# Optimization experiments

Hardware: AMD Instinct MI355X
Metric: run time of the kernel (lower is better)

Reference implementation:

```python
import jax, jax.numpy as jnp
import numpy as np

GX, GY, NH = 480, 360, 32
EPS = 1e-5


def _bn(x, g, b):
    # torch BatchNorm1d training-mode stats over the point dimension
    m = jnp.mean(x, axis=0)
    v = jnp.mean((x - m) ** 2, axis=0)
    return g * (x - m) / jnp.sqrt(v + EPS) + b


def setup_inputs():
    key = jax.random.key(0)
    ks = jax.random.split(key, 24)
    B, N, F = 2, 120000, 7
    s = 0.02
    inp = {
        "pt_fea": jax.random.normal(ks[0], (B, N, F), jnp.float32),
        "xy_ind": jax.random.randint(ks[1], (B, N, 2), 0, 360, dtype=jnp.int32),
        "bn0_g": jnp.ones((7,), jnp.float32), "bn0_b": jnp.zeros((7,), jnp.float32),
        "W1": jax.random.normal(ks[2], (7, 64), jnp.float32) * s,  "b1": jnp.zeros((64,), jnp.float32),
        "bn1_g": jnp.ones((64,), jnp.float32), "bn1_b": jnp.zeros((64,), jnp.float32),
        "W2": jax.random.normal(ks[3], (64, 128), jnp.float32) * s, "b2": jnp.zeros((128,), jnp.float32),
        "bn2_g": jnp.ones((128,), jnp.float32), "bn2_b": jnp.zeros((128,), jnp.float32),
        "W3": jax.random.normal(ks[4], (128, 256), jnp.float32) * s, "b3": jnp.zeros((256,), jnp.float32),
        "bn3_g": jnp.ones((256,), jnp.float32), "bn3_b": jnp.zeros((256,), jnp.float32),
        "W4": jax.random.normal(ks[5], (256, 512), jnp.float32) * s, "b4": jnp.zeros((512,), jnp.float32),
        "W5": jax.random.normal(ks[6], (512, NH), jnp.float32) * s, "b5": jnp.zeros((NH,), jnp.float32),
    }
    return inp


def _forward_sample(fea, xy, bn0_g, bn0_b, W1, b1, bn1_g, bn1_b, W2, b2,
                    bn2_g, bn2_b, W3, b3, bn3_g, bn3_b, W4, b4, W5, b5):
    # Simplified PointNet: BN -> (Linear, BN, ReLU) x3 -> Linear
    x = _bn(fea, bn0_g, bn0_b)
    x = jax.nn.relu(_bn(x @ W1 + b1, bn1_g, bn1_b))
    x = jax.nn.relu(_bn(x @ W2 + b2, bn2_g, bn2_b))
    x = jax.nn.relu(_bn(x @ W3 + b3, bn3_g, bn3_b))
    x = x @ W4 + b4                              # [N, 512]
    # per-voxel segment max over flattened BEV cell id
    ids = xy[:, 0] * GY + xy[:, 1]               # [N]
    nseg = GX * GY
    seg = jax.ops.segment_max(x, ids, num_segments=nseg)   # [nseg, 512]
    cnt = jax.ops.segment_sum(jnp.ones(ids.shape[0], x.dtype), ids, num_segments=nseg)
    occ = (cnt > 0)[:, None]
    seg = jnp.where(occ, seg, 0.0)               # empty voxels -> 0 (scatter semantics)
    nh = jax.nn.relu(seg @ W5 + b5)              # fea_compression
    nh = jnp.where(occ, nh, 0.0)
    return nh.reshape(GX, GY, NH).transpose(2, 0, 1)  # [NH, GX, GY]


def reference(pt_fea, xy_ind, bn0_g, bn0_b, W1, b1, bn1_g, bn1_b, W2, b2,
              bn2_g, bn2_b, W3, b3, bn3_g, bn3_b, W4, b4, W5, b5):
    f = lambda fea, xy: _forward_sample(fea, xy, bn0_g, bn0_b, W1, b1, bn1_g, bn1_b,
                                        W2, b2, bn2_g, bn2_b, W3, b3, bn3_g, bn3_b,
                                        W4, b4, W5, b5)
    return jax.vmap(f)(pt_fea, xy_ind)           # [B, NH, GX, GY]
```

## Files before the change

### kernel.cpp

```cpp
#include <hip/hip_runtime.h>
#include <cstdint>

#define GXD 480
#define GYD 360
#define NHD 32
#define NPTS 120000
#define MPAD 120064
#define SEGR 129600
#define NSEG (GXD*GYD)
#define EPSB 1e-5f

using short8 = __attribute__((ext_vector_type(8))) short;
using f32x4  = __attribute__((ext_vector_type(4))) float;

__device__ __forceinline__ float bf2f(unsigned short u) {
    return __uint_as_float(((unsigned int)u) << 16);
}
__device__ __forceinline__ unsigned short f2bf(float f) {
    unsigned int u = __float_as_uint(f);
    u += 0x7fffu + ((u >> 16) & 1u);
    return (unsigned short)(u >> 16);
}
__device__ __forceinline__ unsigned int bnrelu_pack(unsigned int wv, float sc0, float sh0,
                                                    float sc1, float sh1)
{
    float lo = __uint_as_float(wv << 16);
    float hi = __uint_as_float(wv & 0xffff0000u);
    lo = fmaxf(fmaf(lo, sc0, sh0), 0.f);
    hi = fmaxf(fmaf(hi, sc1, sh1), 0.f);
    unsigned int r;
    asm("v_cvt_pk_bf16_f32 %0, %1, %2" : "=v"(r) : "v"(lo), "v"(hi));
    return r;
}

__device__ __forceinline__ void async16(const unsigned short* g, unsigned short* l)
{
    __builtin_amdgcn_global_load_lds(
        (const __attribute__((address_space(1))) unsigned int*)g,
        (__attribute__((address_space(3))) unsigned int*)l, 16, 0, 0);
}

__global__ __launch_bounds__(256) void bn0_stats_kernel(
    const float* __restrict__ fea, float* __restrict__ s0, float* __restrict__ q0)
{
    float s[7] = {0,0,0,0,0,0,0}, q[7] = {0,0,0,0,0,0,0};
    for (int p = blockIdx.x * 256 + threadIdx.x; p < NPTS; p += gridDim.x * 256) {
        const float* r = fea + (size_t)p * 7;
#pragma unroll
        for (int f = 0; f < 7; ++f) { float v = r[f]; s[f] += v; q[f] += v * v; }
    }
    __shared__ float red[256];
    int t = threadIdx.x;
#pragma unroll
    for (int f = 0; f < 7; ++f) {
        red[t] = s[f]; __syncthreads();
        for (int o = 128; o > 0; o >>= 1) {
            if (t < o) red[t] += red[t + o];
            __syncthreads();
        }
        if (t == 0) atomicAdd(&s0[f], red[0]);
        __syncthreads();
        red[t] = q[f]; __syncthreads();
        for (int o = 128; o > 0; o >>= 1) {
            if (t < o) red[t] += red[t + o];
            __syncthreads();
        }
        if (t == 0) atomicAdd(&q0[f], red[0]);
        __syncthreads();
    }
}

__global__ void prep0_kernel(const float* __restrict__ s0, const float* __restrict__ q0,
                             const float* __restrict__ g0, const float* __restrict__ b0,
                             const float* __restrict__ W1, const float* __restrict__ b1,
                             float* __restrict__ W1p, float* __restrict__ b1p)
{
    __shared__ float sc[7], sh[7];
    int t = threadIdx.x;
    if (t < 7) {
        float m = s0[t] / (float)NPTS;
        float v = q0[t] / (float)NPTS - m * m;
        float inv = 1.0f / sqrtf(fmaxf(v, 0.f) + EPSB);
        sc[t] = g0[t] * inv;
        sh[t] = b0[t] - m * g0[t] * inv;
    }
    __syncthreads();
    if (t < 64) {
        float acc = b1[t];
#pragma unroll
        for (int f = 0; f < 7; ++f) {
            W1p[f * 64 + t] = W1[f * 64 + t] * sc[f];
            acc += sh[f] * W1[f * 64 + t];
        }
        b1p[t] = acc;
    }
}

__global__ void prep_bn_kernel(const float* __restrict__ sum, const float* __restrict__ sq,
                               const float* __restrict__ g, const float* __restrict__ b,
                               float* __restrict__ sc, float* __restrict__ sh, int C)
{
    int c = blockIdx.x * blockDim.x + threadIdx.x;
    if (c < C) {
        float m = sum[c] / (float)NPTS;
        float v = sq[c] / (float)NPTS - m * m;
        float inv = 1.0f / sqrtf(fmaxf(v, 0.f) + EPSB);
        sc[c] = g[c] * inv;
        sh[c] = b[c] - m * g[c] * inv;
    }
}

template<int C>
__global__ __launch_bounds__(256) void bnrelu_kernel(
    unsigned short* __restrict__ Y,
    const float* __restrict__ sc, const float* __restrict__ sh)
{
    __shared__ float scs[C], shs[C];
    int t = threadIdx.x;
    for (int i = t; i < C; i += 256) { scs[i] = sc[i]; shs[i] = sh[i]; }
    __syncthreads();
    const size_t total8 = (size_t)MPAD * C / 8;
    for (size_t i = (size_t)blockIdx.x * 256 + t; i < total8; i += (size_t)gridDim.x * 256) {
        int c0 = (int)((i * 8) & (size_t)(C - 1));
        uint4 v = *(const uint4*)(Y + i * 8);
        float4 s0 = *(const float4*)&scs[c0];
        float4 s1 = *(const float4*)&scs[c0 + 4];
        float4 h0 = *(const float4*)&shs[c0];
        float4 h1 = *(const float4*)&shs[c0 + 4];
        uint4 o;
        o.x = bnrelu_pack(v.x, s0.x, h0.x, s0.y, h0.y);
        o.y = bnrelu_pack(v.y, s0.z, h0.z, s0.w, h0.w);
        o.z = bnrelu_pack(v.z, s1.x, h1.x, s1.y, h1.y);
        o.w = bnrelu_pack(v.w, s1.z, h1.z, s1.w, h1.w);
        *(uint4*)(Y + i * 8) = o;
    }
}

__global__ __launch_bounds__(256) void wtrans_kernel(const float* __restrict__ W,
                                                     unsigned short* __restrict__ Wt,
                                                     int K, int N)
{
    int i = blockIdx.x * 256 + threadIdx.x;
    if (i < K * N) {
        int k = i / N, n = i % N;
        Wt[(size_t)n * K + k] = f2bf(W[i]);
    }
}

__global__ __launch_bounds__(256) void layer1_kernel(
    const float* __restrict__ fea, const float* __restrict__ W1p, const float* __restrict__ b1p,
    unsigned short* __restrict__ y1, float* __restrict__ sum1, float* __restrict__ sq1)
{
    __shared__ float Wl[448], bl[64];
    __shared__ float feaL[256 * 7];
    __shared__ float colsum[64], colsq[64];
    int t = threadIdx.x;
    int p0 = blockIdx.x * 256;
    for (int i = t; i < 448; i += 256) Wl[i] = W1p[i];
    if (t < 64) { bl[t] = b1p[t]; colsum[t] = 0.f; colsq[t] = 0.f; }
    int nval7 = (NPTS - p0) * 7;
    for (int i = t; i < 256 * 7; i += 256)
        feaL[i] = (i < nval7) ? fea[(size_t)p0 * 7 + i] : 0.f;
    __syncthreads();
    int cg = t & 7, pt = t >> 3;
    float s[8] = {}, q[8] = {};
#pragma unroll
    for (int it = 0; it < 8; ++it) {
        int row = it * 32 + pt;
        bool valid = (p0 + row) < NPTS;
        float f[7];
#pragma unroll
        for (int ff = 0; ff < 7; ++ff) f[ff] = feaL[row * 7 + ff];
        float vj[8];
#pragma unroll
        for (int j = 0; j < 8; ++j) {
            int c = cg * 8 + j;
            float v = bl[c];
#pragma unroll
            for (int ff = 0; ff < 7; ++ff) v = fmaf(f[ff], Wl[ff * 64 + c], v);
            vj[j] = v;
            if (valid) { s[j] += v; q[j] += v * v; }
        }
        uint4 ow;
        ow.x = (unsigned int)f2bf(vj[0]) | ((unsigned int)f2bf(vj[1]) << 16);
        ow.y = (unsigned int)f2bf(vj[2]) | ((unsigned int)f2bf(vj[3]) << 16);
        ow.z = (unsigned int)f2bf(vj[4]) | ((unsigned int)f2bf(vj[5]) << 16);
        ow.w = (unsigned int)f2bf(vj[6]) | ((unsigned int)f2bf(vj[7]) << 16);
        *(uint4*)(y1 + (size_t)(p0 + row) * 64 + cg * 8) = ow;
    }
#pragma unroll
    for (int off = 8; off < 64; off <<= 1) {
#pragma unroll
        for (int j = 0; j < 8; ++j) {
            s[j] += __shfl_xor(s[j], off);
            q[j] += __shfl_xor(q[j], off);
        }
    }
    if ((t & 63) < 8) {
#pragma unroll
        for (int j = 0; j < 8; ++j) {
            atomicAdd(&colsum[cg * 8 + j], s[j]);
            atomicAdd(&colsq[cg * 8 + j], q[j]);
        }
    }
    __syncthreads();
    if (t < 64) {
        atomicAdd(&sum1[t], colsum[t]);
        atomicAdd(&sq1[t], colsq[t]);
    }
}

template<int K, int NC, bool STATS>
__global__ __launch_bounds__(256) void gemm_quad(
    const unsigned short* __restrict__ A, const unsigned short* __restrict__ Wt,
    const float* __restrict__ bias, unsigned short* __restrict__ Y,
    float* __restrict__ osum, float* __restrict__ osq)
{
    __shared__ __align__(16) unsigned short lds[16384];
    __shared__ float colsum[128], colsq[128];
    int t = threadIdx.x;
    int w = t >> 6, ln = t & 63, quad = ln >> 4, lr = ln & 15;
    int wr = w >> 1, wc = w & 1;
    const int mbase = blockIdx.y * 128;
    const int cbase = blockIdx.x * 128;
    unsigned short* Asl = lds;
    unsigned short* Bsl = lds + 8192;

    if (STATS && t < 128) { colsum[t] = 0.f; colsq[t] = 0.f; }
    __syncthreads();

    const int srow = w * 16 + (ln >> 2);
    const int koff = (ln & 3) * 8;

    auto stage = [&](int buf, int kt) {
#pragma unroll
        for (int half = 0; half < 2; ++half) {
            int row = half * 64 + srow;
            async16(A  + (size_t)(mbase + row) * K + kt + koff,
                    Asl + buf * 4096 + half * 2048 + w * 512 + ln * 8);
            async16(Wt + (size_t)(cbase + row) * K + kt + koff,
                    Bsl + buf * 4096 + half * 2048 + w * 512 + ln * 8);
        }
    };

    f32x4 acc[4][4];
#pragma unroll
    for (int i = 0; i < 4; ++i)
#pragma unroll
        for (int j = 0; j < 4; ++j) acc[i][j] = (f32x4){0.f, 0.f, 0.f, 0.f};

    stage(0, 0);
    stage(1, 32);

    constexpr int NR = K / 32;
#pragma unroll
    for (int r = 0; r < NR; ++r) {
        const int buf = r & 1;
        if (r + 1 < NR)
            asm volatile("s_waitcnt vmcnt(4)" ::: "memory");
        else
            asm volatile("s_waitcnt vmcnt(0)" ::: "memory");
        asm volatile("s_barrier" ::: "memory");
        short8 af[4], bfr[4];
#pragma unroll
        for (int mi = 0; mi < 4; ++mi)
            af[mi] = *(const short8*)&Asl[buf * 4096 + (wr * 64 + mi * 16 + lr) * 32 + quad * 8];
#pragma unroll
        for (int ni = 0; ni < 4; ++ni)
            bfr[ni] = *(const short8*)&Bsl[buf * 4096 + (wc * 64 + ni * 16 + lr) * 32 + quad * 8];
        asm volatile("s_waitcnt lgkmcnt(0)" ::: "memory");
        asm volatile("s_barrier" ::: "memory");
        if (r + 2 < NR)
            stage(buf, (r + 2) * 32);
#pragma unroll
        for (int mi = 0; mi < 4; ++mi)
#pragma unroll
            for (int ni = 0; ni < 4; ++ni)
                acc[mi][ni] = __builtin_amdgcn_mfma_f32_16x16x32_bf16(
                    af[mi], bfr[ni], acc[mi][ni], 0, 0, 0);
    }
    __syncthreads();

    unsigned short* Cw = lds + w * 4096;
#pragma unroll
    for (int ni = 0; ni < 4; ++ni) {
        int col = ni * 16 + lr;
        float bv = bias[cbase + wc * 64 + col];
        float s = 0.f, q = 0.f;
#pragma unroll
        for (int mi = 0; mi < 4; ++mi) {
            int rb = mi * 16 + quad * 4;
#pragma unroll
            for (int r = 0; r < 4; ++r) {
                float v = acc[mi][ni][r] + bv;
                Cw[(rb + r) * 64 + col] = f2bf(v);
                if (STATS && (mbase + wr * 64 + rb + r) < NPTS) { s += v; q += v * v; }
            }
        }
        if (STATS) {
            atomicAdd(&colsum[wc * 64 + col], s);
            atomicAdd(&colsq[wc * 64 + col], q);
        }
    }
#pragma unroll
    for (int i = 0; i < 8; ++i) {
        int idx = i * 64 + ln;
        int row = idx >> 3, colq = (idx & 7) * 8;
        *(uint4*)(Y + (size_t)(mbase + wr * 64 + row) * NC + cbase + wc * 64 + colq) =
            *(const uint4*)&Cw[row * 64 + colq];
    }
    if (STATS) {
        __syncthreads();
        if (t < 128) {
            atomicAdd(&osum[blockIdx.x * 128 + t], colsum[t]);
            atomicAdd(&osq[blockIdx.x * 128 + t], colsq[t]);
        }
    }
}

__global__ __launch_bounds__(256) void hist_kernel(const int* __restrict__ xy,
                                                   int* __restrict__ cnt)
{
    int p = blockIdx.x * 256 + threadIdx.x;
    if (p < NPTS) {
        int id = xy[(size_t)p * 2] * GYD + xy[(size_t)p * 2 + 1];
        atomicAdd(&cnt[id], 1);
    }
}

__global__ __launch_bounds__(256) void scanA_kernel(const int* __restrict__ cnt,
                                                    int* __restrict__ csum)
{
    __shared__ int red[256];
    int t = threadIdx.x, base = blockIdx.x * 2048;
    int s = 0;
    for (int i = t; i < 2048; i += 256) {
        int idx = base + i;
        if (idx < SEGR) s += cnt[idx];
    }
    red[t] = s; __syncthreads();
    for (int o = 128; o > 0; o >>= 1) { if (t < o) red[t] += red[t + o]; __syncthreads(); }
    if (t == 0) csum[blockIdx.x] = red[0];
}

__global__ void scanB_kernel(int* __restrict__ csum, int* __restrict__ offs)
{
    if (threadIdx.x == 0) {
        int run = 0;
        for (int i = 0; i < 64; ++i) { int v = csum[i]; csum[i] = run; run += v; }
        offs[SEGR] = run;
    }
}

__global__ __launch_bounds__(256) void scanC_kernel(const int* __restrict__ cnt,
                                                    const int* __restrict__ csum,
                                                    int* __restrict__ offs,
                                                    int* __restrict__ cursor)
{
    __shared__ int red[256];
    int t = threadIdx.x, base = blockIdx.x * 2048;
    int v[8]; int s = 0;
#pragma unroll
    for (int i = 0; i < 8; ++i) {
        int idx = base + t * 8 + i;
        v[i] = (idx < SEGR) ? cnt[idx] : 0;
        s += v[i];
    }
    red[t] = s; __syncthreads();
    for (int o = 1; o < 256; o <<= 1) {
        int x = (t >= o) ? red[t - o] : 0;
        __syncthreads();
        red[t] += x;
        __syncthreads();
    }
    int run = red[t] - s + csum[blockIdx.x];
#pragma unroll
    for (int i = 0; i < 8; ++i) {
        int idx = base + t * 8 + i;
        if (idx < SEGR) { offs[idx] = run; cursor[idx] = run; }
        run += v[i];
    }
}

__global__ __launch_bounds__(256) void scatter_idx_kernel(const int* __restrict__ xy,
                                                          int* __restrict__ cursor,
                                                          int* __restrict__ order)
{
    int p = blockIdx.x * 256 + threadIdx.x;
    if (p < NPTS) {
        int id = xy[(size_t)p * 2] * GYD + xy[(size_t)p * 2 + 1];
        int pos = atomicAdd(&cursor[id], 1);
        order[pos] = p;
    }
}

__global__ __launch_bounds__(256) void segmax_l5_kernel(
    const unsigned short* __restrict__ y4g, const unsigned short* __restrict__ Wt5,
    const int* __restrict__ offs, const int* __restrict__ order,
    int g, float* __restrict__ E)
{
    __shared__ __align__(16) unsigned short seg[64 * 136];
    __shared__ __align__(16) unsigned short w5s[32 * 136];
    __shared__ int offs_s[65];
    int t = threadIdx.x;
    int c0 = blockIdx.x * 64;
    if (t < 65) offs_s[t] = offs[c0 + t];
    {
        int n = t >> 3, ko = (t & 7) * 16;
        *(uint4*)&w5s[n * 136 + ko]     = *(const uint4*)(Wt5 + (size_t)n * 512 + g * 128 + ko);
        *(uint4*)&w5s[n * 136 + ko + 8] = *(const uint4*)(Wt5 + (size_t)n * 512 + g * 128 + ko + 8);
    }
    __syncthreads();
    int cell = t >> 2, q = t & 3;
    float mx[32];
#pragma unroll
    for (int i = 0; i < 32; ++i) mx[i] = -3.0e38f;
    int jb = offs_s[cell], je = offs_s[cell + 1];
    for (int j = jb; j < je; ++j) {
        int p = order[j];
        const uint4* rp = (const uint4*)(y4g + (size_t)p * 128 + q * 32);
#pragma unroll
        for (int u = 0; u < 4; ++u) {
            uint4 vv = rp[u];
            unsigned int wv[4] = {vv.x, vv.y, vv.z, vv.w};
#pragma unroll
            for (int k2 = 0; k2 < 4; ++k2) {
                int idx = u * 8 + k2 * 2;
                mx[idx]     = fmaxf(mx[idx],     bf2f((unsigned short)(wv[k2] & 0xffffu)));
                mx[idx + 1] = fmaxf(mx[idx + 1], bf2f((unsigned short)(wv[k2] >> 16)));
            }
        }
    }
    bool empty = (jb == je);
#pragma unroll
    for (int i = 0; i < 16; ++i) {
        float lo = empty ? 0.f : mx[2 * i], hi = empty ? 0.f : mx[2 * i + 1];
        unsigned int pk = (unsigned int)f2bf(lo) | ((unsigned int)f2bf(hi) << 16);
        *(unsigned int*)&seg[cell * 136 + q * 32 + 2 * i] = pk;
    }
    __syncthreads();
    int lane = t & 63, w = t >> 6, quad = lane >> 4, lr = lane & 15;
    f32x4 acc[2];
    acc[0] = (f32x4){0.f, 0.f, 0.f, 0.f};
    acc[1] = (f32x4){0.f, 0.f, 0.f, 0.f};
#pragma unroll
    for (int kt = 0; kt < 4; ++kt) {
        short8 af = *(const short8*)&seg[(w * 16 + lr) * 136 + kt * 32 + quad * 8];
#pragma unroll
        for (int ni = 0; ni < 2; ++ni) {
            short8 bfr = *(const short8*)&w5s[(ni * 16 + lr) * 136 + kt * 32 + quad * 8];
            acc[ni] = __builtin_amdgcn_mfma_f32_16x16x32_bf16(af, bfr, acc[ni], 0, 0, 0);
        }
    }
#pragma unroll
    for (int ni = 0; ni < 2; ++ni) {
        int h = ni * 16 + lr;
#pragma unroll
        for (int r = 0; r < 4; ++r) {
            int cr = w * 16 + quad * 4 + r;
            float* ep = E + (size_t)(c0 + cr) * 32 + h;
            float v = acc[ni][r];
            if (g > 0) v += *ep;
            *ep = v;
        }
    }
}

__global__ __launch_bounds__(256) void out_kernel(
    const float* __restrict__ E, const int* __restrict__ cnt,
    const float* __restrict__ b5, float* __restrict__ out)
{
    int t = threadIdx.x;
    int c0 = blockIdx.x * 64;
    int lane = t & 63, hq = t >> 6;
    int cell = c0 + lane;
    if (c0 >= SEGR) {
#pragma unroll
        for (int j = 0; j < 8; ++j)
            out[(size_t)(hq * 8 + j) * NSEG + cell] = 0.f;
        return;
    }
    bool oc = cnt[cell] > 0;
    float4 e0 = *(const float4*)(E + (size_t)cell * 32 + hq * 8);
    float4 e1 = *(const float4*)(E + (size_t)cell * 32 + hq * 8 + 4);
    float r[8] = {e0.x, e0.y, e0.z, e0.w, e1.x, e1.y, e1.z, e1.w};
#pragma unroll
    for (int j = 0; j < 8; ++j) {
        float v = oc ? fmaxf(r[j] + b5[hq * 8 + j], 0.f) : 0.f;
        out[(size_t)(hq * 8 + j) * NSEG + cell] = v;
    }
}

extern "C" void kernel_launch(void* const* d_in, const int* in_sizes, int n_in,
                              void* d_out, int out_size, void* d_ws, size_t ws_size,
                              hipStream_t stream)
{
    const float* pt_fea = (const float*)d_in[0];
    const int*   xy_ind = (const int*)d_in[1];
    const float* bn0_g  = (const float*)d_in[2];
    const float* bn0_b  = (const float*)d_in[3];
    const float* W1     = (const float*)d_in[4];
    const float* b1     = (const float*)d_in[5];
    const float* bn1_g  = (const float*)d_in[6];
    const float* bn1_b  = (const float*)d_in[7];
    const float* W2     = (const float*)d_in[8];
    const float* b2     = (const float*)d_in[9];
    const float* bn2_g  = (const float*)d_in[10];
    const float* bn2_b  = (const float*)d_in[11];
    const float* W3     = (const float*)d_in[12];
    const float* b3     = (const float*)d_in[13];
    const float* bn3_g  = (const float*)d_in[14];
    const float* bn3_b  = (const float*)d_in[15];
    const float* W4     = (const float*)d_in[16];
    const float* b4     = (const float*)d_in[17];
    const float* W5     = (const float*)d_in[18];
    const float* b5     = (const float*)d_in[19];
    float* out = (float*)d_out;

    const size_t oY2   = 61472768;
    const size_t oE    = oY2 + (size_t)MPAD * 128 * 2;
    const size_t oCnt  = oE + (size_t)SEGR * 32 * 4;
    const size_t oOffs = oCnt + 518400;
    const size_t oCur  = oOffs + 518528;
    const size_t oOrd  = oCur + 518400;
    const size_t oCsum = oOrd + 480000;
    const size_t oSt   = oCsum + 512;
    const size_t oWt2  = oSt + 16384;
    const size_t oWt3  = oWt2 + 16384;
    const size_t oWt4  = oWt3 + 65536;
    const size_t oWt5  = oWt4 + 262144;

    unsigned short* y1   = (unsigned short*)d_ws;
    unsigned short* y3   = (unsigned short*)d_ws;
    unsigned short* y2   = (unsigned short*)((char*)d_ws + oY2);
    unsigned short* y4g  = (unsigned short*)((char*)d_ws + oY2);
    float*          E    = (float*)((char*)d_ws + oE);
    int*            cnt  = (int*)((char*)d_ws + oCnt);
    int*            offs = (int*)((char*)d_ws + oOffs);
    int*            cur  = (int*)((char*)d_ws + oCur);
    int*            ord  = (int*)((char*)d_ws + oOrd);
    int*            csum = (int*)((char*)d_ws + oCsum);
    float*          st   = (float*)((char*)d_ws + oSt);
    unsigned short* Wt2  = (unsigned short*)((char*)d_ws + oWt2);
    unsigned short* Wt3  = (unsigned short*)((char*)d_ws + oWt3);
    unsigned short* Wt4  = (unsigned short*)((char*)d_ws + oWt4);
    unsigned short* Wt5  = (unsigned short*)((char*)d_ws + oWt5);

    float* s0 = st + 0;     float* q0 = st + 8;
    float* W1p = st + 16;   float* b1p = st + 464;
    float* sum1 = st + 528; float* sq1 = st + 592; float* sc1 = st + 656; float* sh1 = st + 720;
    float* sum2 = st + 784; float* sq2 = st + 912; float* sc2 = st + 1040; float* sh2 = st + 1168;
    float* sum3 = st + 1296; float* sq3 = st + 1552; float* sc3 = st + 1808; float* sh3 = st + 2064;

    const int MB128 = MPAD / 128;

    wtrans_kernel<<<(64 * 128 + 255) / 256, 256, 0, stream>>>(W2, Wt2, 64, 128);
    wtrans_kernel<<<(128 * 256 + 255) / 256, 256, 0, stream>>>(W3, Wt3, 128, 256);
    wtrans_kernel<<<(256 * 512 + 255) / 256, 256, 0, stream>>>(W4, Wt4, 256, 512);
    wtrans_kernel<<<(512 * 32 + 255) / 256, 256, 0, stream>>>(W5, Wt5, 512, 32);

    for (int b = 0; b < 2; ++b) {
        const float* fea_b = pt_fea + (size_t)b * NPTS * 7;
        const int*   xy_b  = xy_ind + (size_t)b * NPTS * 2;
        float*       out_b = out + (size_t)b * NHD * NSEG;

        (void)hipMemsetAsync(st, 0, 2320 * sizeof(float), stream);
        (void)hipMemsetAsync(cnt, 0, (size_t)SEGR * 4, stream);

        bn0_stats_kernel<<<128, 256, 0, stream>>>(fea_b, s0, q0);
        prep0_kernel<<<1, 64, 0, stream>>>(s0, q0, bn0_g, bn0_b, W1, b1, W1p, b1p);
        layer1_kernel<<<MPAD / 256, 256, 0, stream>>>(fea_b, W1p, b1p, y1, sum1, sq1);
        prep_bn_kernel<<<1, 64, 0, stream>>>(sum1, sq1, bn1_g, bn1_b, sc1, sh1, 64);
        bnrelu_kernel<64><<<1024, 256, 0, stream>>>(y1, sc1, sh1);
        gemm_quad<64, 128, true><<<dim3(1, MB128), 256, 0, stream>>>(
            y1, Wt2, b2, y2, sum2, sq2);
        prep_bn_kernel<<<1, 128, 0, stream>>>(sum2, sq2, bn2_g, bn2_b, sc2, sh2, 128);
        bnrelu_kernel<128><<<2048, 256, 0, stream>>>(y2, sc2, sh2);
        gemm_quad<128, 256, true><<<dim3(2, MB128), 256, 0, stream>>>(
            y2, Wt3, b3, y3, sum3, sq3);
        prep_bn_kernel<<<1, 256, 0, stream>>>(sum3, sq3, bn3_g, bn3_b, sc3, sh3, 256);
        bnrelu_kernel<256><<<2048, 256, 0, stream>>>(y3, sc3, sh3);

        hist_kernel<<<(NPTS + 255) / 256, 256, 0, stream>>>(xy_b, cnt);
        scanA_kernel<<<64, 256, 0, stream>>>(cnt, csum);
        scanB_kernel<<<1, 64, 0, stream>>>(csum, offs);
        scanC_kernel<<<64, 256, 0, stream>>>(cnt, csum, offs, cur);
        scatter_idx_kernel<<<(NPTS + 255) / 256, 256, 0, stream>>>(xy_b, cur, ord);

        for (int g = 0; g < 4; ++g) {
            gemm_quad<256, 128, false><<<dim3(1, MB128), 256, 0, stream>>>(
                y3, Wt4 + (size_t)g * 128 * 256, b4 + g * 128, y4g,
                nullptr, nullptr);
            segmax_l5_kernel<<<SEGR / 64, 256, 0, stream>>>(y4g, Wt5, offs, ord, g, E);
        }
        out_kernel<<<NSEG / 64, 256, 0, stream>>>(E, cnt, b5, out_b);
    }
}
```

Before: 809.2 us.

## Add persistent multi-tile GEMM with resident weights and 3-slab async A pipeline

Adds a gemm_ml kernel that keeps the full weight slice for a 64-column block resident in LDS and loops persistently over many 128-row M tiles. A is streamed through a three-slab ring of async loads, so the next tile's A prefetch overlaps the current MMA and epilogue. It replaces gemm_quad for layer 3 and the four W4 chunk GEMMs, using fixed 256-row-block grids. The goal is to stop reloading weights per tile and to hide global load latency. In exchange it adds hand-written waitcnt/barrier sequencing that is fragile, a narrower 64-column output tile, and possibly lower occupancy.

```diff
diff --git a/kernel.cpp b/kernel.cpp
--- a/kernel.cpp
+++ b/kernel.cpp
@@ -6,6 +6,7 @@
 #define NHD 32
 #define NPTS 120000
 #define MPAD 120064
+#define MB128 (MPAD/128)
 #define SEGR 129600
 #define NSEG (GXD*GYD)
 #define EPSB 1e-5f
@@ -314,6 +315,139 @@
         if (t < 128) {
             atomicAdd(&osum[blockIdx.x * 128 + t], colsum[t]);
             atomicAdd(&osq[blockIdx.x * 128 + t], colsq[t]);
+        }
+    }
+}
+
+template<int K, int NC, bool STATS>
+__global__ __launch_bounds__(256) void gemm_ml(
+    const unsigned short* __restrict__ A, const unsigned short* __restrict__ Wt,
+    const float* __restrict__ bias, unsigned short* __restrict__ Y,
+    float* __restrict__ osum, float* __restrict__ osq)
+{
+    constexpr int NR = K / 32;
+    __shared__ __align__(16) unsigned short Bsl[NR * 2048];
+    __shared__ __align__(16) unsigned short Asl[3 * 4096];
+    __shared__ float colsum[64], colsq[64];
+    int t = threadIdx.x;
+    int w = t >> 6, ln = t & 63, quad = ln >> 4, lr = ln & 15;
+    int wr = w >> 1, wc = w & 1;
+    const int cbase = blockIdx.x * 64;
+    const int by = blockIdx.y, NB = gridDim.y;
+    const int nt = 1 + (MB128 - 1 - by) / NB;
+
+    if (STATS && t < 64) { colsum[t] = 0.f; colsq[t] = 0.f; }
+
+    const int srow = w * 16 + (ln >> 2);
+    const int koff = (ln & 3) * 8;
+
+#pragma unroll
+    for (int r = 0; r < NR; ++r)
+        async16(Wt + (size_t)(cbase + srow) * K + r * 32 + koff,
+                Bsl + r * 2048 + w * 512 + ln * 8);
+
+    auto stageA = [&](int slab, int mbs, int r) {
+#pragma unroll
+        for (int half = 0; half < 2; ++half)
+            async16(A + (size_t)(mbs + half * 64 + srow) * K + r * 32 + koff,
+                    Asl + slab * 4096 + half * 2048 + w * 512 + ln * 8);
+    };
+
+    int mb = by * 128;
+    stageA(0, mb, 0);
+    stageA(1, mb, 1);
+
+    f32x4 acc[4][2];
+#pragma unroll
+    for (int i = 0; i < 4; ++i) {
+        acc[i][0] = (f32x4){0.f, 0.f, 0.f, 0.f};
+        acc[i][1] = (f32x4){0.f, 0.f, 0.f, 0.f};
+    }
+
+    int slab = 0;
+    for (int i = 0; i < nt; ++i) {
+        mb = (by + i * NB) * 128;
+        const int mbn = (by + (i + 1) * NB) * 128;
+        const bool lastt = (i == nt - 1);
+#pragma unroll
+        for (int r = 0; r < NR; ++r) {
+            if (r == 0) {
+                if (i == 0) {
+                    asm volatile("s_waitcnt vmcnt(2)" ::: "memory");
+                    asm volatile("s_barrier" ::: "memory");
+                }
+            } else {
+                if (lastt && r == NR - 1)
+                    asm volatile("s_waitcnt vmcnt(0)" ::: "memory");
+                else
+                    asm volatile("s_waitcnt vmcnt(2)" ::: "memory");
+                asm volatile("s_barrier" ::: "memory");
+            }
+            int s2 = slab + 2; if (s2 >= 3) s2 -= 3;
+            if (r + 2 < NR)                 stageA(s2, mb, r + 2);
+            else if (r == NR - 2 && !lastt) stageA(s2, mbn, 0);
+            short8 af[4], bfr[2];
+#pragma unroll
+            for (int mi = 0; mi < 4; ++mi)
+                af[mi] = *(const short8*)&Asl[slab * 4096 + wr * 2048 + (mi * 16 + lr) * 32 + quad * 8];
+#pragma unroll
+            for (int ni = 0; ni < 2; ++ni)
+                bfr[ni] = *(const short8*)&Bsl[r * 2048 + (wc * 32 + ni * 16 + lr) * 32 + quad * 8];
+            asm volatile("s_waitcnt lgkmcnt(0)" ::: "memory");
+#pragma unroll
+            for (int mi = 0; mi < 4; ++mi)
+#pragma unroll
+                for (int ni = 0; ni < 2; ++ni)
+                    acc[mi][ni] = __builtin_amdgcn_mfma_f32_16x16x32_bf16(
+                        af[mi], bfr[ni], acc[mi][ni], 0, 0, 0);
+            ++slab; if (slab == 3) slab = 0;
+        }
+        int cs = slab + 1; if (cs >= 3) cs -= 3;
+#pragma unroll
+        for (int ni = 0; ni < 2; ++ni) {
+            int col = wc * 32 + ni * 16 + lr;
+            float bv = bias[cbase + col];
+            float s = 0.f, q = 0.f;
+#pragma unroll
+            for (int mi = 0; mi < 4; ++mi)
+#pragma unroll
+                for (int rr = 0; rr < 4; ++rr) {
+                    float v = acc[mi][ni][rr] + bv;
+                    acc[mi][ni][rr] = v;
+                    if (STATS && (mb + wr * 64 + mi * 16 + quad * 4 + rr) < NPTS) { s += v; q += v * v; }
+                }
+            if (STATS) { atomicAdd(&colsum[col], s); atomicAdd(&colsq[col], q); }
+        }
+        unsigned short* strip = Asl + cs * 4096 + w * 512;
+#pragma unroll
+        for (int mi = 0; mi < 4; ++mi) {
+#pragma unroll
+            for (int ni = 0; ni < 2; ++ni)
+#pragma unroll
+                for (int rr = 0; rr < 4; ++rr) {
+                    int row = quad * 4 + rr;
+                    int c = (ni * 16 + lr) ^ (quad << 3);
+                    strip[row * 32 + c] = f2bf(acc[mi][ni][rr]);
+                }
+            int row = ln >> 2, colq = (ln & 3) * 8;
+            int colq2 = colq ^ ((row >> 2) << 3);
+            uint4 vv = *(const uint4*)&strip[row * 32 + colq2];
+            *(uint4*)(Y + (size_t)(mb + wr * 64 + mi * 16 + row) * NC + cbase + wc * 32 + colq) = vv;
+        }
+        asm volatile("s_waitcnt vmcnt(4)" ::: "memory");
+        asm volatile("s_barrier" ::: "memory");
+        if (!lastt) stageA(cs, mbn, 1);
+#pragma unroll
+        for (int mi = 0; mi < 4; ++mi) {
+            acc[mi][0] = (f32x4){0.f, 0.f, 0.f, 0.f};
+            acc[mi][1] = (f32x4){0.f, 0.f, 0.f, 0.f};
+        }
+    }
+    if (STATS) {
+        __syncthreads();
+        if (t < 64) {
+            atomicAdd(&osum[cbase + t], colsum[t]);
+            atomicAdd(&osq[cbase + t], colsq[t]);
         }
     }
 }
@@ -552,8 +686,6 @@
     float* sum2 = st + 784; float* sq2 = st + 912; float* sc2 = st + 1040; float* sh2 = st + 1168;
     float* sum3 = st + 1296; float* sq3 = st + 1552; float* sc3 = st + 1808; float* sh3 = st + 2064;
 
-    const int MB128 = MPAD / 128;
-
     wtrans_kernel<<<(64 * 128 + 255) / 256, 256, 0, stream>>>(W2, Wt2, 64, 128);
     wtrans_kernel<<<(128 * 256 + 255) / 256, 256, 0, stream>>>(W3, Wt3, 128, 256);
     wtrans_kernel<<<(256 * 512 + 255) / 256, 256, 0, stream>>>(W4, Wt4, 256, 512);
@@ -576,7 +708,7 @@
             y1, Wt2, b2, y2, sum2, sq2);
         prep_bn_kernel<<<1, 128, 0, stream>>>(sum2, sq2, bn2_g, bn2_b, sc2, sh2, 128);
         bnrelu_kernel<128><<<2048, 256, 0, stream>>>(y2, sc2, sh2);
-        gemm_quad<128, 256, true><<<dim3(2, MB128), 256, 0, stream>>>(
+        gemm_ml<128, 256, true><<<dim3(4, 256), 256, 0, stream>>>(
             y2, Wt3, b3, y3, sum3, sq3);
         prep_bn_kernel<<<1, 256, 0, stream>>>(sum3, sq3, bn3_g, bn3_b, sc3, sh3, 256);
         bnrelu_kernel<256><<<2048, 256, 0, stream>>>(y3, sc3, sh3);
@@ -588,7 +720,7 @@
         scatter_idx_kernel<<<(NPTS + 255) / 256, 256, 0, stream>>>(xy_b, cur, ord);
 
         for (int g = 0; g < 4; ++g) {
-            gemm_quad<256, 128, false><<<dim3(1, MB128), 256, 0, stream>>>(
+            gemm_ml<256, 128, false><<<dim3(2, 256), 256, 0, stream>>>(
                 y3, Wt4 + (size_t)g * 128 * 256, b4 + g * 128, y4g,
                 nullptr, nullptr);
             segmax_l5_kernel<<<SEGR / 64, 256, 0, stream>>>(y4g, Wt5, offs, ord, g, E);
```

After: 903.1 us. +11.6%, slower.

## Fuse layer-4 GEMM, segment max, and compression into one per-cell-block kernel

Applied to the files above, without the earlier changes.

Replaces the four-pass loop (layer-4 GEMM writing y4 to global, then a segmax+layer-5 kernel accumulating into E) and the separate output kernel with one kernel. Each block owns 64 cells, gathers its points' y3 rows in sorted order, computes layer 4 on the fly into LDS with double-buffered async loads, takes the per-cell max, and applies W5, bias and ReLU directly to the output. Blocks whose cells are all empty write zeros and exit, and a small tail kernel zeroes cells beyond SEGR. This removes the round trips of the 512-wide layer-4 activations and E through global memory. In exchange it uses gathered A rows, partially filled 64-row tiles, and recomputes W4 loads per block.

```diff
diff --git a/kernel.cpp b/kernel.cpp
--- a/kernel.cpp
+++ b/kernel.cpp
@@ -6,6 +6,7 @@
 #define NHD 32
 #define NPTS 120000
 #define MPAD 120064
+#define MB128 (MPAD/128)
 #define SEGR 129600
 #define NSEG (GXD*GYD)
 #define EPSB 1e-5f
@@ -394,101 +395,154 @@
     }
 }
 
-__global__ __launch_bounds__(256) void segmax_l5_kernel(
-    const unsigned short* __restrict__ y4g, const unsigned short* __restrict__ Wt5,
-    const int* __restrict__ offs, const int* __restrict__ order,
-    int g, float* __restrict__ E)
-{
-    __shared__ __align__(16) unsigned short seg[64 * 136];
+__global__ __launch_bounds__(256) void l4seg_kernel(
+    const unsigned short* __restrict__ y3, const unsigned short* __restrict__ Wt4,
+    const float* __restrict__ b4, const unsigned short* __restrict__ Wt5,
+    const float* __restrict__ b5, const int* __restrict__ offs,
+    const int* __restrict__ ord, float* __restrict__ out)
+{
+    __shared__ __align__(16) unsigned short Asl[2][2048];
+    __shared__ __align__(16) unsigned short Bsl[2][4096];
+    __shared__ __align__(16) unsigned short y4s[64 * 136];
     __shared__ __align__(16) unsigned short w5s[32 * 136];
+    __shared__ float b4s[128];
     __shared__ int offs_s[65];
     int t = threadIdx.x;
+    int w = t >> 6, ln = t & 63, quad = ln >> 4, lr = ln & 15;
     int c0 = blockIdx.x * 64;
     if (t < 65) offs_s[t] = offs[c0 + t];
-    {
-        int n = t >> 3, ko = (t & 7) * 16;
-        *(uint4*)&w5s[n * 136 + ko]     = *(const uint4*)(Wt5 + (size_t)n * 512 + g * 128 + ko);
-        *(uint4*)&w5s[n * 136 + ko + 8] = *(const uint4*)(Wt5 + (size_t)n * 512 + g * 128 + ko + 8);
-    }
-    __syncthreads();
-    int cell = t >> 2, q = t & 3;
-    float mx[32];
-#pragma unroll
-    for (int i = 0; i < 32; ++i) mx[i] = -3.0e38f;
-    int jb = offs_s[cell], je = offs_s[cell + 1];
-    for (int j = jb; j < je; ++j) {
-        int p = order[j];
-        const uint4* rp = (const uint4*)(y4g + (size_t)p * 128 + q * 32);
-#pragma unroll
-        for (int u = 0; u < 4; ++u) {
-            uint4 vv = rp[u];
-            unsigned int wv[4] = {vv.x, vv.y, vv.z, vv.w};
-#pragma unroll
-            for (int k2 = 0; k2 < 4; ++k2) {
-                int idx = u * 8 + k2 * 2;
-                mx[idx]     = fmaxf(mx[idx],     bf2f((unsigned short)(wv[k2] & 0xffffu)));
-                mx[idx + 1] = fmaxf(mx[idx + 1], bf2f((unsigned short)(wv[k2] >> 16)));
+    __syncthreads();
+    const int jb = offs_s[0], je = offs_s[64];
+    if (jb == je) {
+#pragma unroll
+        for (int j = 0; j < 8; ++j)
+            out[(size_t)(w * 8 + j) * NSEG + c0 + ln] = 0.f;
+        return;
+    }
+    const int cell = t >> 2, q = t & 3;
+    const int cjb = offs_s[cell], cje = offs_s[cell + 1];
+
+    f32x4 eacc[2];
+    eacc[0] = (f32x4){0.f, 0.f, 0.f, 0.f};
+    eacc[1] = (f32x4){0.f, 0.f, 0.f, 0.f};
+
+    const int srow = w * 16 + (ln >> 2);
+    const int koff = (ln & 3) * 8;
+
+    for (int g = 0; g < 4; ++g) {
+        {
+            int n = t >> 3, ko = (t & 7) * 16;
+            *(uint4*)&w5s[n * 136 + ko]     = *(const uint4*)(Wt5 + (size_t)n * 512 + g * 128 + ko);
+            *(uint4*)&w5s[n * 136 + ko + 8] = *(const uint4*)(Wt5 + (size_t)n * 512 + g * 128 + ko + 8);
+            if (t < 128) b4s[t] = b4[g * 128 + t];
+        }
+        float mxv[32];
+#pragma unroll
+        for (int i = 0; i < 32; ++i) mxv[i] = -3.0e38f;
+
+        const unsigned short* Bg = Wt4 + (size_t)(g * 128 + srow) * 256 + koff;
+
+        for (int cs = jb; cs < je; cs += 64) {
+            int aj = cs + srow; if (aj >= je) aj = je - 1;
+            const unsigned short* Ag = y3 + (size_t)ord[aj] * 256 + koff;
+            auto stage = [&](int buf, int r) {
+                async16(Ag + r * 32,            &Asl[buf][0] + w * 512 + ln * 8);
+                async16(Bg + r * 32,            &Bsl[buf][0] + w * 512 + ln * 8);
+                async16(Bg + 64 * 256 + r * 32, &Bsl[buf][2048] + w * 512 + ln * 8);
+            };
+            f32x4 acc[8];
+#pragma unroll
+            for (int i = 0; i < 8; ++i) acc[i] = (f32x4){0.f, 0.f, 0.f, 0.f};
+            stage(0, 0); stage(1, 1);
+#pragma unroll
+            for (int r = 0; r < 8; ++r) {
+                if (r < 7) asm volatile("s_waitcnt vmcnt(3)" ::: "memory");
+                else       asm volatile("s_waitcnt vmcnt(0)" ::: "memory");
+                asm volatile("s_barrier" ::: "memory");
+                const int buf = r & 1;
+                short8 af = *(const short8*)&Asl[buf][(w * 16 + lr) * 32 + quad * 8];
+                short8 bfr[8];
+#pragma unroll
+                for (int ni = 0; ni < 8; ++ni)
+                    bfr[ni] = *(const short8*)&Bsl[buf][(ni * 16 + lr) * 32 + quad * 8];
+                asm volatile("s_waitcnt lgkmcnt(0)" ::: "memory");
+                asm volatile("s_barrier" ::: "memory");
+                if (r + 2 < 8) stage(buf, r + 2);
+#pragma unroll
+                for (int ni = 0; ni < 8; ++ni)
+                    acc[ni] = __builtin_amdgcn_mfma_f32_16x16x32_bf16(af, bfr[ni], acc[ni], 0, 0, 0);
             }
-        }
-    }
-    bool empty = (jb == je);
-#pragma unroll
-    for (int i = 0; i < 16; ++i) {
-        float lo = empty ? 0.f : mx[2 * i], hi = empty ? 0.f : mx[2 * i + 1];
-        unsigned int pk = (unsigned int)f2bf(lo) | ((unsigned int)f2bf(hi) << 16);
-        *(unsigned int*)&seg[cell * 136 + q * 32 + 2 * i] = pk;
-    }
-    __syncthreads();
-    int lane = t & 63, w = t >> 6, quad = lane >> 4, lr = lane & 15;
-    f32x4 acc[2];
-    acc[0] = (f32x4){0.f, 0.f, 0.f, 0.f};
-    acc[1] = (f32x4){0.f, 0.f, 0.f, 0.f};
-#pragma unroll
-    for (int kt = 0; kt < 4; ++kt) {
-        short8 af = *(const short8*)&seg[(w * 16 + lr) * 136 + kt * 32 + quad * 8];
-#pragma unroll
-        for (int ni = 0; ni < 2; ++ni) {
-            short8 bfr = *(const short8*)&w5s[(ni * 16 + lr) * 136 + kt * 32 + quad * 8];
-            acc[ni] = __builtin_amdgcn_mfma_f32_16x16x32_bf16(af, bfr, acc[ni], 0, 0, 0);
-        }
-    }
+#pragma unroll
+            for (int ni = 0; ni < 8; ++ni) {
+                float bv = b4s[ni * 16 + lr];
+#pragma unroll
+                for (int rr = 0; rr < 4; ++rr)
+                    y4s[(w * 16 + quad * 4 + rr) * 136 + ni * 16 + lr] = f2bf(acc[ni][rr] + bv);
+            }
+            __syncthreads();
+            int lo = cjb > cs ? cjb : cs;
+            int hi = cje < cs + 64 ? cje : cs + 64;
+            for (int j = lo; j < hi; ++j) {
+                const uint4* rp = (const uint4*)&y4s[(j - cs) * 136 + q * 32];
+#pragma unroll
+                for (int u = 0; u < 4; ++u) {
+                    uint4 vv = rp[u];
+                    unsigned int wv[4] = {vv.x, vv.y, vv.z, vv.w};
+#pragma unroll
+                    for (int k2 = 0; k2 < 4; ++k2) {
+                        int idx = u * 8 + k2 * 2;
+                        mxv[idx]     = fmaxf(mxv[idx],     bf2f((unsigned short)(wv[k2] & 0xffffu)));
+                        mxv[idx + 1] = fmaxf(mxv[idx + 1], bf2f((unsigned short)(wv[k2] >> 16)));
+                    }
+                }
+            }
+            __syncthreads();
+        }
+        {
+            bool empty = (cjb == cje);
+#pragma unroll
+            for (int i = 0; i < 16; ++i) {
+                float lo2 = empty ? 0.f : mxv[2 * i], hi2 = empty ? 0.f : mxv[2 * i + 1];
+                unsigned int pk = (unsigned int)f2bf(lo2) | ((unsigned int)f2bf(hi2) << 16);
+                *(unsigned int*)&y4s[cell * 136 + q * 32 + 2 * i] = pk;
+            }
+        }
+        __syncthreads();
+#pragma unroll
+        for (int kt = 0; kt < 4; ++kt) {
+            short8 af = *(const short8*)&y4s[(w * 16 + lr) * 136 + kt * 32 + quad * 8];
+#pragma unroll
+            for (int ni = 0; ni < 2; ++ni) {
+                short8 bfr = *(const short8*)&w5s[(ni * 16 + lr) * 136 + kt * 32 + quad * 8];
+                eacc[ni] = __builtin_amdgcn_mfma_f32_16x16x32_bf16(af, bfr, eacc[ni], 0, 0, 0);
+            }
+        }
+        __syncthreads();
+    }
+    float* outs = (float*)&Asl[0][0];
 #pragma unroll
     for (int ni = 0; ni < 2; ++ni) {
         int h = ni * 16 + lr;
-#pragma unroll
-        for (int r = 0; r < 4; ++r) {
-            int cr = w * 16 + quad * 4 + r;
-            float* ep = E + (size_t)(c0 + cr) * 32 + h;
-            float v = acc[ni][r];
-            if (g > 0) v += *ep;
-            *ep = v;
-        }
-    }
-}
-
-__global__ __launch_bounds__(256) void out_kernel(
-    const float* __restrict__ E, const int* __restrict__ cnt,
-    const float* __restrict__ b5, float* __restrict__ out)
-{
-    int t = threadIdx.x;
-    int c0 = blockIdx.x * 64;
-    int lane = t & 63, hq = t >> 6;
-    int cell = c0 + lane;
-    if (c0 >= SEGR) {
-#pragma unroll
-        for (int j = 0; j < 8; ++j)
-            out[(size_t)(hq * 8 + j) * NSEG + cell] = 0.f;
-        return;
-    }
-    bool oc = cnt[cell] > 0;
-    float4 e0 = *(const float4*)(E + (size_t)cell * 32 + hq * 8);
-    float4 e1 = *(const float4*)(E + (size_t)cell * 32 + hq * 8 + 4);
-    float r[8] = {e0.x, e0.y, e0.z, e0.w, e1.x, e1.y, e1.z, e1.w};
-#pragma unroll
-    for (int j = 0; j < 8; ++j) {
-        float v = oc ? fmaxf(r[j] + b5[hq * 8 + j], 0.f) : 0.f;
-        out[(size_t)(hq * 8 + j) * NSEG + cell] = v;
-    }
+        float bv = b5[h];
+#pragma unroll
+        for (int rr = 0; rr < 4; ++rr) {
+            int cr = w * 16 + quad * 4 + rr;
+            bool oc = offs_s[cr + 1] > offs_s[cr];
+            outs[cr * 33 + h] = oc ? fmaxf(eacc[ni][rr] + bv, 0.f) : 0.f;
+        }
+    }
+    __syncthreads();
+#pragma unroll
+    for (int j = 0; j < 8; ++j)
+        out[(size_t)(w * 8 + j) * NSEG + c0 + ln] = outs[ln * 33 + w * 8 + j];
+}
+
+__global__ __launch_bounds__(256) void ztail_kernel(float* __restrict__ out)
+{
+    int i = blockIdx.x * 256 + threadIdx.x;
+    const int per = (NSEG - SEGR) / 4;
+    int h = i / per, c = i % per;
+    *(float4*)(out + (size_t)h * NSEG + SEGR + (size_t)c * 4) = make_float4(0.f, 0.f, 0.f, 0.f);
 }
 
 extern "C" void kernel_launch(void* const* d_in, const int* in_sizes, int n_in,
@@ -533,8 +587,6 @@
     unsigned short* y1   = (unsigned short*)d_ws;
     unsigned short* y3   = (unsigned short*)d_ws;
     unsigned short* y2   = (unsigned short*)((char*)d_ws + oY2);
-    unsigned short* y4g  = (unsigned short*)((char*)d_ws + oY2);
-    float*          E    = (float*)((char*)d_ws + oE);
     int*            cnt  = (int*)((char*)d_ws + oCnt);
     int*            offs = (int*)((char*)d_ws + oOffs);
     int*            cur  = (int*)((char*)d_ws + oCur);
@@ -551,8 +603,6 @@
     float* sum1 = st + 528; float* sq1 = st + 592; float* sc1 = st + 656; float* sh1 = st + 720;
     float* sum2 = st + 784; float* sq2 = st + 912; float* sc2 = st + 1040; float* sh2 = st + 1168;
     float* sum3 = st + 1296; float* sq3 = st + 1552; float* sc3 = st + 1808; float* sh3 = st + 2064;
-
-    const int MB128 = MPAD / 128;
 
     wtrans_kernel<<<(64 * 128 + 255) / 256, 256, 0, stream>>>(W2, Wt2, 64, 128);
     wtrans_kernel<<<(128 * 256 + 255) / 256, 256, 0, stream>>>(W3, Wt3, 128, 256);
@@ -587,12 +637,7 @@
         scanC_kernel<<<64, 256, 0, stream>>>(cnt, csum, offs, cur);
         scatter_idx_kernel<<<(NPTS + 255) / 256, 256, 0, stream>>>(xy_b, cur, ord);
 
-        for (int g = 0; g < 4; ++g) {
-            gemm_quad<256, 128, false><<<dim3(1, MB128), 256, 0, stream>>>(
-                y3, Wt4 + (size_t)g * 128 * 256, b4 + g * 128, y4g,
-                nullptr, nullptr);
-            segmax_l5_kernel<<<SEGR / 64, 256, 0, stream>>>(y4g, Wt5, offs, ord, g, E);
-        }
-        out_kernel<<<NSEG / 64, 256, 0, stream>>>(E, cnt, b5, out_b);
-    }
-}
+        l4seg_kernel<<<SEGR / 64, 256, 0, stream>>>(y3, Wt4, b4, Wt5, b5, offs, ord, out_b);
+        ztail_kernel<<<1350, 256, 0, stream>>>(out_b);
+    }
+}
```

Result: slower. 834.6 us (+3.1%).
